# Kernel optimization log

Hardware: AMD Instinct MI355X
Metric: run time of the kernel (lower is better)

The kernel has to match this reference:

```python
import jax, jax.numpy as jnp
import numpy as np

B, MC, U, N, DIN, DOUT, E = 2048, 4, 20000, 100000, 128, 128, 65536
RES_RATE = 0.9


def setup_inputs() -> dict:
    key = jax.random.key(0)
    ks = jax.random.split(key, 12)
    s = 1.0 / np.sqrt(DIN)
    return {
        'nodes': jax.random.randint(ks[0], (B,), 0, N),
        'unique_ids': jax.random.randint(ks[1], (U,), 0, N),
        'row_idx': jnp.repeat(jnp.arange(B), E // B),
        'layer_idx': jax.random.randint(ks[2], (E,), 0, MC),
        'col_idx': jax.random.randint(ks[3], (E,), 0, U),
        'agg_table': jax.random.normal(ks[4], (N, DIN), jnp.float32),
        'ff_table': jax.random.normal(ks[5], (N, DIN), jnp.float32),
        'Wv_agg': jax.random.normal(ks[6], (DIN, DOUT), jnp.float32) * s,
        'Wv_ff': jax.random.normal(ks[7], (DIN, DOUT), jnp.float32) * s,
        'Wk': jax.random.normal(ks[8], (DIN, DOUT), jnp.float32) * s,
        'Wq': jax.random.normal(ks[9], (DIN, DOUT), jnp.float32) * s,
        'mu_w': jax.random.normal(ks[10], (2 * DOUT, 1), jnp.float32) * s,
    }


def reference(nodes, unique_ids, row_idx, layer_idx, col_idx,
              agg_table, ff_table, Wv_agg, Wv_ff, Wk, Wq, mu_w):
    # feature lookups (the 'features' encoder returns (agg_attr, ff_attr))
    embed_agg = agg_table[unique_ids]            # [U, DIN]
    self_agg_raw = agg_table[nodes]              # [B, DIN]
    self_ff_raw = ff_table[nodes]                # [B, DIN]

    # highway K/Q from raw self features
    self_pair = jnp.stack((self_agg_raw, self_ff_raw), axis=1)  # [B, 2, DIN]
    K = self_pair @ Wk                            # [B, 2, DOUT]
    Q = self_pair @ Wq                            # [B, 2, DOUT]

    embed_agg_v = embed_agg @ Wv_agg              # [U, DOUT]
    self_agg = self_agg_raw @ Wv_agg              # [B, DOUT]

    # dense normalized neighbor mask [B, MC, U]
    mask = jnp.zeros((B, MC, U), jnp.float32).at[row_idx, layer_idx, col_idx].set(1.0)
    cnt = mask.sum(-1, keepdims=True)
    mask = mask / jnp.where(cnt == 0, 1.0, cnt)
    neigh = jnp.einsum('bmu,ud->bmd', mask, embed_agg_v)  # [B, MC, DOUT]

    # persona combination
    coef = jnp.concatenate(
        (jnp.broadcast_to(self_agg[:, None, :], (B, MC, DOUT)), neigh), axis=-1)
    norm = jnp.maximum(jnp.linalg.norm(coef, axis=-1, keepdims=True), 1e-12)
    coef = jax.nn.softmax((coef / norm) @ mu_w, axis=1)    # [B, MC, 1]
    neigh_sum = jnp.sum(neigh * coef, axis=1)              # [B, DOUT]
    self_agg = (self_agg + neigh_sum) / 2.0

    # feed-forward branch + highway attention
    self_ff = self_ff_raw @ Wv_ff                          # [B, DOUT]
    V = jnp.stack((self_agg, self_ff), axis=1)             # [B, 2, DOUT]
    scores = jax.nn.softmax(jnp.einsum('bid,bjd->bij', K, Q) / DOUT, axis=-1)
    new = jnp.einsum('bij,bjd->bid', scores, V)            # [B, 2, DOUT]
    self_agg = RES_RATE * self_agg + (1 - RES_RATE) * new[:, 0]
    self_ff = RES_RATE * self_ff + (1 - RES_RATE) * new[:, 1]
    return jax.nn.elu(self_agg), jax.nn.elu(self_ff)
```

## Files before the change

kernel.cpp:

```cpp
#include <hip/hip_runtime.h>
#include <hip/hip_bf16.h>

typedef unsigned short u16;
typedef unsigned int u32;
typedef unsigned long long u64;

#define NB 2048
#define NMC 4
#define NU 20000
#define ND 128
#define EPB 32

typedef __attribute__((ext_vector_type(8))) short bf16x8;
typedef __attribute__((ext_vector_type(4))) float f32x4;

__device__ __forceinline__ u32 pack_bf16(float a, float b) {
    __hip_bfloat162 h = __float22bfloat162_rn(make_float2(a, b));
    return *(u32*)&h;
}
__device__ __forceinline__ u16 f2bf(float f) {
    u32 x = __float_as_uint(f);
    return (u16)((x + 0x7fffu + ((x >> 16) & 1u)) >> 16);
}
__device__ __forceinline__ float wsum(float v) {
    #pragma unroll
    for (int off = 32; off; off >>= 1) v += __shfl_xor(v, off);
    return v;
}

__global__ __launch_bounds__(256) void prep_wt(
    const float* __restrict__ Wv_agg, const float* __restrict__ Wk,
    const float* __restrict__ Wq, const float* __restrict__ Wv_ff,
    u16* __restrict__ WT)
{
    __shared__ float Wl[16 * ND];
    const int m = blockIdx.x >> 3;
    const int ks = (blockIdx.x & 7) * 16;
    const int t = threadIdx.x;

    const float* W = (m == 0) ? Wv_agg : (m == 1) ? Wk : (m == 2) ? Wq : Wv_ff;
    const float4* src = (const float4*)(W + ks * ND);
    float4* dst = (float4*)Wl;
    dst[t * 2] = src[t * 2];
    dst[t * 2 + 1] = src[t * 2 + 1];
    __syncthreads();

    const int c = t >> 1, kh = t & 1;
    float v[8];
    #pragma unroll
    for (int j = 0; j < 8; j++) v[j] = Wl[(kh * 8 + j) * ND + c];
    uint4 pk;
    pk.x = pack_bf16(v[0], v[1]);
    pk.y = pack_bf16(v[2], v[3]);
    pk.z = pack_bf16(v[4], v[5]);
    pk.w = pack_bf16(v[6], v[7]);
    *(uint4*)&WT[((size_t)(m * ND + c)) * ND + ks + kh * 8] = pk;
}

#define LDSK 72
#define EMBED_BLOCKS 157

__global__ __launch_bounds__(256) void gemm_all(
    const float* __restrict__ agg, const float* __restrict__ ff,
    const u16* __restrict__ WT,
    const int* __restrict__ uids, const int* __restrict__ nodes,
    u16* __restrict__ embed_bf,
    float* __restrict__ selfA, float* __restrict__ selfF,
    float* __restrict__ K0, float* __restrict__ K1,
    float* __restrict__ Q0, float* __restrict__ Q1)
{
    __shared__ u16 As[ND * LDSK];
    __shared__ u16 Bs[ND * LDSK];

    const int bx = blockIdx.x;
    const int t  = threadIdx.x;

    const float* table = agg; const int* ids = uids; int wtm = 0;
    float* outf = nullptr; u16* outb = nullptr;
    int M, r0;
    if (bx < EMBED_BLOCKS) {
        M = NU; r0 = bx * 128; outb = embed_bf;
    } else {
        int z = bx - EMBED_BLOCKS;
        int mode = z >> 4;
        r0 = (z & 15) * 128;
        M = NB; ids = nodes;
        switch (mode) {
            case 0: table = agg; wtm = 0; outf = selfA; break;
            case 1: table = agg; wtm = 1; outf = K0;    break;
            case 2: table = agg; wtm = 2; outf = Q0;    break;
            case 3: table = ff;  wtm = 3; outf = selfF; break;
            case 4: table = ff;  wtm = 1; outf = K1;    break;
            default: table = ff; wtm = 2; outf = Q1;    break;
        }
    }

    const int rs = t >> 1, hs = t & 1;
    int srow = r0 + rs;
    const int id = ids[srow < M ? srow : (M - 1)];
    const float* arow = table + (size_t)id * ND;
    const u16* wrow = WT + ((size_t)(wtm * ND + rs)) * ND;

    const int w = t >> 6, lane = t & 63, q = lane >> 4, li = lane & 15;

    f32x4 acc[2][8];
    #pragma unroll
    for (int i = 0; i < 2; i++)
        #pragma unroll
        for (int j = 0; j < 8; j++) acc[i][j] = (f32x4){0.f, 0.f, 0.f, 0.f};

    for (int pass = 0; pass < 2; pass++) {
        const int k0 = pass * 64;
        {
            const float4* asrc = (const float4*)(arow + k0 + hs * 32);
            #pragma unroll
            for (int i = 0; i < 4; i++) {
                float4 v0 = asrc[2 * i], v1 = asrc[2 * i + 1];
                uint4 pk;
                pk.x = pack_bf16(v0.x, v0.y);
                pk.y = pack_bf16(v0.z, v0.w);
                pk.z = pack_bf16(v1.x, v1.y);
                pk.w = pack_bf16(v1.z, v1.w);
                *(uint4*)&As[rs * LDSK + hs * 32 + i * 8] = pk;
            }
        }
        {
            const uint4* bsrc = (const uint4*)(wrow + k0 + hs * 32);
            #pragma unroll
            for (int i = 0; i < 4; i++)
                *(uint4*)&Bs[rs * LDSK + hs * 32 + i * 8] = bsrc[i];
        }
        __syncthreads();

        #pragma unroll
        for (int c = 0; c < 2; c++) {
            const int kk = c * 32 + q * 8;
            bf16x8 af[2], bfr[8];
            #pragma unroll
            for (int tr = 0; tr < 2; tr++)
                af[tr] = *(const bf16x8*)&As[(w * 32 + tr * 16 + li) * LDSK + kk];
            #pragma unroll
            for (int tc = 0; tc < 8; tc++)
                bfr[tc] = *(const bf16x8*)&Bs[(tc * 16 + li) * LDSK + kk];
            #pragma unroll
            for (int tr = 0; tr < 2; tr++)
                #pragma unroll
                for (int tc = 0; tc < 8; tc++)
                    acc[tr][tc] = __builtin_amdgcn_mfma_f32_16x16x32_bf16(
                        af[tr], bfr[tc], acc[tr][tc], 0, 0, 0);
        }
        __syncthreads();
    }

    #pragma unroll
    for (int tr = 0; tr < 2; tr++) {
        const int rloc = w * 32 + tr * 16 + q * 4;
        #pragma unroll
        for (int r = 0; r < 4; r++) {
            const int row = r0 + rloc + r;
            if (row < M) {
                if (outb) {
                    #pragma unroll
                    for (int tc = 0; tc < 8; tc++)
                        outb[(size_t)row * ND + tc * 16 + li] = f2bf(acc[tr][tc][r]);
                } else {
                    #pragma unroll
                    for (int tc = 0; tc < 8; tc++)
                        outf[(size_t)row * ND + tc * 16 + li] = acc[tr][tc][r];
                }
            }
        }
    }
}

__global__ __launch_bounds__(64) void finalize(
    const int* __restrict__ layer_idx, const int* __restrict__ col_idx,
    const u16* __restrict__ embed_bf,
    const float* __restrict__ selfA, const float* __restrict__ selfF,
    const float* __restrict__ K0, const float* __restrict__ K1,
    const float* __restrict__ Q0, const float* __restrict__ Q1,
    const float* __restrict__ mu_w, float* __restrict__ out)
{
    const int b = blockIdx.x;
    const int t = threadIdx.x;

    int l = 0, c = 0;
    if (t < EPB) {
        l = layer_idx[b * EPB + t];
        c = col_idx[b * EPB + t];
    }
    const u32 key = ((u32)l << 15) | (u32)c;
    int dup = 0;
    #pragma unroll
    for (int j = 0; j < EPB; j++) {
        u32 kj = __shfl(key, j);
        dup |= (j < t && kj == key);
    }
    const int keep = (t < EPB) && !dup;
    float inv[NMC];
    #pragma unroll
    for (int m = 0; m < NMC; m++) {
        int cm = __popcll(__ballot(keep && (l == m)));
        inv[m] = cm > 0 ? 1.f / (float)cm : 0.f;
    }
    const u32 info = ((u32)c << 3) | ((u32)l << 1) | (u32)keep;

    float a0x = 0.f, a0y = 0.f, a1x = 0.f, a1y = 0.f;
    float a2x = 0.f, a2y = 0.f, a3x = 0.f, a3y = 0.f;
    #pragma unroll
    for (int e = 0; e < EPB; e++) {
        u32 inf = __shfl(info, e);
        if (inf & 1u) {
            int ce = inf >> 3, le = (inf >> 1) & 3;
            u32 v = *(const u32*)&embed_bf[(size_t)ce * ND + 2 * t];
            float lo = __uint_as_float(v << 16);
            float hi = __uint_as_float(v & 0xffff0000u);
            switch (le) {
                case 0: a0x += lo; a0y += hi; break;
                case 1: a1x += lo; a1y += hi; break;
                case 2: a2x += lo; a2y += hi; break;
                default: a3x += lo; a3y += hi; break;
            }
        }
    }
    const float n0x = a0x * inv[0], n0y = a0y * inv[0];
    const float n1x = a1x * inv[1], n1y = a1y * inv[1];
    const float n2x = a2x * inv[2], n2y = a2y * inv[2];
    const float n3x = a3x * inv[3], n3y = a3y * inv[3];

    const size_t base2 = (size_t)b * ND + 2 * t;
    float2 sA = *(const float2*)&selfA[base2];
    float2 sF = *(const float2*)&selfF[base2];
    float2 k0 = *(const float2*)&K0[base2];
    float2 k1 = *(const float2*)&K1[base2];
    float2 q0 = *(const float2*)&Q0[base2];
    float2 q1 = *(const float2*)&Q1[base2];
    float2 mu0 = *(const float2*)&mu_w[2 * t];
    float2 mu1 = *(const float2*)&mu_w[ND + 2 * t];

    const float sn = wsum(sA.x * sA.x + sA.y * sA.y);
    const float ds = wsum(sA.x * mu0.x + sA.y * mu0.y);
    float nn[NMC], dn[NMC];
    nn[0] = wsum(n0x * n0x + n0y * n0y); dn[0] = wsum(n0x * mu1.x + n0y * mu1.y);
    nn[1] = wsum(n1x * n1x + n1y * n1y); dn[1] = wsum(n1x * mu1.x + n1y * mu1.y);
    nn[2] = wsum(n2x * n2x + n2y * n2y); dn[2] = wsum(n2x * mu1.x + n2y * mu1.y);
    nn[3] = wsum(n3x * n3x + n3y * n3y); dn[3] = wsum(n3x * mu1.x + n3y * mu1.y);
    const float s00 = wsum(k0.x * q0.x + k0.y * q0.y) * (1.f / 128.f);
    const float s01 = wsum(k0.x * q1.x + k0.y * q1.y) * (1.f / 128.f);
    const float s10 = wsum(k1.x * q0.x + k1.y * q0.y) * (1.f / 128.f);
    const float s11 = wsum(k1.x * q1.x + k1.y * q1.y) * (1.f / 128.f);

    float sc[NMC], mx = -1e30f;
    #pragma unroll
    for (int m = 0; m < NMC; m++) {
        float nrm = fmaxf(sqrtf(sn + nn[m]), 1e-12f);
        sc[m] = (ds + dn[m]) / nrm;
        mx = fmaxf(mx, sc[m]);
    }
    float se = 0.f, ee[NMC];
    #pragma unroll
    for (int m = 0; m < NMC; m++) { ee[m] = expf(sc[m] - mx); se += ee[m]; }
    const float ise = 1.f / se;
    const float bc0 = ee[0] * ise, bc1 = ee[1] * ise;
    const float bc2 = ee[2] * ise, bc3 = ee[3] * ise;

    const float m0 = fmaxf(s00, s01), e00 = expf(s00 - m0), e01 = expf(s01 - m0);
    const float id0 = 1.f / (e00 + e01);
    const float c00 = e00 * id0, c01 = e01 * id0;
    const float m1 = fmaxf(s10, s11), e10 = expf(s10 - m1), e11 = expf(s11 - m1);
    const float id1 = 1.f / (e10 + e11);
    const float c10 = e10 * id1, c11 = e11 * id1;

    const float nsx = n0x * bc0 + n1x * bc1 + n2x * bc2 + n3x * bc3;
    const float nsy = n0y * bc0 + n1y * bc1 + n2y * bc2 + n3y * bc3;
    const float sa1x = (sA.x + nsx) * 0.5f, sa1y = (sA.y + nsy) * 0.5f;
    float o0x = 0.9f * sa1x + 0.1f * (c00 * sa1x + c01 * sF.x);
    float o0y = 0.9f * sa1y + 0.1f * (c00 * sa1y + c01 * sF.y);
    float o1x = 0.9f * sF.x + 0.1f * (c10 * sa1x + c11 * sF.x);
    float o1y = 0.9f * sF.y + 0.1f * (c10 * sa1y + c11 * sF.y);
    o0x = o0x > 0.f ? o0x : (expf(o0x) - 1.f);
    o0y = o0y > 0.f ? o0y : (expf(o0y) - 1.f);
    o1x = o1x > 0.f ? o1x : (expf(o1x) - 1.f);
    o1y = o1y > 0.f ? o1y : (expf(o1y) - 1.f);
    *(float2*)&out[base2] = make_float2(o0x, o0y);
    *(float2*)&out[(size_t)NB * ND + base2] = make_float2(o1x, o1y);
}

extern "C" void kernel_launch(void* const* d_in, const int* in_sizes, int n_in,
                              void* d_out, int out_size, void* d_ws, size_t ws_size,
                              hipStream_t stream) {
    const int* nodes  = (const int*)d_in[0];
    const int* uids   = (const int*)d_in[1];
    const int* layer  = (const int*)d_in[3];
    const int* col    = (const int*)d_in[4];
    const float* agg    = (const float*)d_in[5];
    const float* ff     = (const float*)d_in[6];
    const float* Wv_agg = (const float*)d_in[7];
    const float* Wv_ff  = (const float*)d_in[8];
    const float* Wk     = (const float*)d_in[9];
    const float* Wq     = (const float*)d_in[10];
    const float* mu     = (const float*)d_in[11];

    u16*   WT       = (u16*)d_ws;
    u16*   embed_bf = WT + (size_t)4 * ND * ND;
    float* fbase    = (float*)(embed_bf + (size_t)NU * ND);
    float* selfA = fbase;
    float* selfF = selfA + (size_t)NB * ND;
    float* K0    = selfF + (size_t)NB * ND;
    float* K1    = K0 + (size_t)NB * ND;
    float* Q0    = K1 + (size_t)NB * ND;
    float* Q1    = Q0 + (size_t)NB * ND;

    float* out = (float*)d_out;

    prep_wt<<<32, 256, 0, stream>>>(Wv_agg, Wk, Wq, Wv_ff, WT);

    gemm_all<<<EMBED_BLOCKS + 6 * (NB / 128), 256, 0, stream>>>(
        agg, ff, WT, uids, nodes,
        embed_bf, selfA, selfF, K0, K1, Q0, Q1);

    finalize<<<NB, 64, 0, stream>>>(
        layer, col, embed_bf, selfA, selfF, K0, K1, Q0, Q1, mu, out);
}
```

Measured before the change: 153.2 us.

## Fuse weight transpose into GEMM and load A fragments directly into registers

```diff
diff --git a/kernel.cpp b/kernel.cpp
--- a/kernel.cpp
+++ b/kernel.cpp
@@ -3,13 +3,13 @@
 
 typedef unsigned short u16;
 typedef unsigned int u32;
-typedef unsigned long long u64;
 
 #define NB 2048
 #define NMC 4
 #define NU 20000
 #define ND 128
 #define EPB 32
+#define LDW 136
 
 typedef __attribute__((ext_vector_type(8))) short bf16x8;
 typedef __attribute__((ext_vector_type(4))) float f32x4;
@@ -28,54 +28,24 @@
     return v;
 }
 
-__global__ __launch_bounds__(256) void prep_wt(
-    const float* __restrict__ Wv_agg, const float* __restrict__ Wk,
-    const float* __restrict__ Wq, const float* __restrict__ Wv_ff,
-    u16* __restrict__ WT)
-{
-    __shared__ float Wl[16 * ND];
-    const int m = blockIdx.x >> 3;
-    const int ks = (blockIdx.x & 7) * 16;
-    const int t = threadIdx.x;
-
-    const float* W = (m == 0) ? Wv_agg : (m == 1) ? Wk : (m == 2) ? Wq : Wv_ff;
-    const float4* src = (const float4*)(W + ks * ND);
-    float4* dst = (float4*)Wl;
-    dst[t * 2] = src[t * 2];
-    dst[t * 2 + 1] = src[t * 2 + 1];
-    __syncthreads();
-
-    const int c = t >> 1, kh = t & 1;
-    float v[8];
-    #pragma unroll
-    for (int j = 0; j < 8; j++) v[j] = Wl[(kh * 8 + j) * ND + c];
-    uint4 pk;
-    pk.x = pack_bf16(v[0], v[1]);
-    pk.y = pack_bf16(v[2], v[3]);
-    pk.z = pack_bf16(v[4], v[5]);
-    pk.w = pack_bf16(v[6], v[7]);
-    *(uint4*)&WT[((size_t)(m * ND + c)) * ND + ks + kh * 8] = pk;
-}
-
-#define LDSK 72
 #define EMBED_BLOCKS 157
 
 __global__ __launch_bounds__(256) void gemm_all(
     const float* __restrict__ agg, const float* __restrict__ ff,
-    const u16* __restrict__ WT,
+    const float* __restrict__ Wv_agg, const float* __restrict__ Wv_ff,
+    const float* __restrict__ Wk, const float* __restrict__ Wq,
     const int* __restrict__ uids, const int* __restrict__ nodes,
     u16* __restrict__ embed_bf,
     float* __restrict__ selfA, float* __restrict__ selfF,
     float* __restrict__ K0, float* __restrict__ K1,
     float* __restrict__ Q0, float* __restrict__ Q1)
 {
-    __shared__ u16 As[ND * LDSK];
-    __shared__ u16 Bs[ND * LDSK];
+    __shared__ u16 WTl[ND * LDW];
 
     const int bx = blockIdx.x;
     const int t  = threadIdx.x;
 
-    const float* table = agg; const int* ids = uids; int wtm = 0;
+    const float* table = agg; const int* ids = uids; const float* W = Wv_agg;
     float* outf = nullptr; u16* outb = nullptr;
     int M, r0;
     if (bx < EMBED_BLOCKS) {
@@ -86,22 +56,55 @@
         r0 = (z & 15) * 128;
         M = NB; ids = nodes;
         switch (mode) {
-            case 0: table = agg; wtm = 0; outf = selfA; break;
-            case 1: table = agg; wtm = 1; outf = K0;    break;
-            case 2: table = agg; wtm = 2; outf = Q0;    break;
-            case 3: table = ff;  wtm = 3; outf = selfF; break;
-            case 4: table = ff;  wtm = 1; outf = K1;    break;
-            default: table = ff; wtm = 2; outf = Q1;    break;
-        }
-    }
-
-    const int rs = t >> 1, hs = t & 1;
-    int srow = r0 + rs;
-    const int id = ids[srow < M ? srow : (M - 1)];
-    const float* arow = table + (size_t)id * ND;
-    const u16* wrow = WT + ((size_t)(wtm * ND + rs)) * ND;
+            case 0: table = agg; W = Wv_agg; outf = selfA; break;
+            case 1: table = agg; W = Wk;     outf = K0;    break;
+            case 2: table = agg; W = Wq;     outf = Q0;    break;
+            case 3: table = ff;  W = Wv_ff;  outf = selfF; break;
+            case 4: table = ff;  W = Wk;     outf = K1;    break;
+            default: table = ff; W = Wq;     outf = Q1;    break;
+        }
+    }
+
+    {
+        const int kr = t >> 1;
+        const int nh = t & 1;
+        const float4* wsrc = (const float4*)(W + kr * ND + nh * 64);
+        #pragma unroll
+        for (int i = 0; i < 16; i++) {
+            float4 v = wsrc[i];
+            int n = nh * 64 + i * 4;
+            WTl[(n + 0) * LDW + kr] = f2bf(v.x);
+            WTl[(n + 1) * LDW + kr] = f2bf(v.y);
+            WTl[(n + 2) * LDW + kr] = f2bf(v.z);
+            WTl[(n + 3) * LDW + kr] = f2bf(v.w);
+        }
+    }
 
     const int w = t >> 6, lane = t & 63, q = lane >> 4, li = lane & 15;
+    const int rbase = r0 + w * 32;
+    int ra = rbase + li;      ra = ra < M ? ra : M - 1;
+    int rb = rbase + 16 + li; rb = rb < M ? rb : M - 1;
+    const float* arow0 = table + (size_t)ids[ra] * ND + q * 8;
+    const float* arow1 = table + (size_t)ids[rb] * ND + q * 8;
+
+    bf16x8 af[2][4];
+    #pragma unroll
+    for (int c = 0; c < 4; c++) {
+        float4 v0 = *(const float4*)(arow0 + c * 32);
+        float4 v1 = *(const float4*)(arow0 + c * 32 + 4);
+        uint4 pk;
+        pk.x = pack_bf16(v0.x, v0.y); pk.y = pack_bf16(v0.z, v0.w);
+        pk.z = pack_bf16(v1.x, v1.y); pk.w = pack_bf16(v1.z, v1.w);
+        af[0][c] = *(bf16x8*)&pk;
+        float4 u0 = *(const float4*)(arow1 + c * 32);
+        float4 u1 = *(const float4*)(arow1 + c * 32 + 4);
+        uint4 qk;
+        qk.x = pack_bf16(u0.x, u0.y); qk.y = pack_bf16(u0.z, u0.w);
+        qk.z = pack_bf16(u1.x, u1.y); qk.w = pack_bf16(u1.z, u1.w);
+        af[1][c] = *(bf16x8*)&qk;
+    }
+
+    __syncthreads();
 
     f32x4 acc[2][8];
     #pragma unroll
@@ -109,47 +112,21 @@
         #pragma unroll
         for (int j = 0; j < 8; j++) acc[i][j] = (f32x4){0.f, 0.f, 0.f, 0.f};
 
-    for (int pass = 0; pass < 2; pass++) {
-        const int k0 = pass * 64;
-        {
-            const float4* asrc = (const float4*)(arow + k0 + hs * 32);
-            #pragma unroll
-            for (int i = 0; i < 4; i++) {
-                float4 v0 = asrc[2 * i], v1 = asrc[2 * i + 1];
-                uint4 pk;
-                pk.x = pack_bf16(v0.x, v0.y);
-                pk.y = pack_bf16(v0.z, v0.w);
-                pk.z = pack_bf16(v1.x, v1.y);
-                pk.w = pack_bf16(v1.z, v1.w);
-                *(uint4*)&As[rs * LDSK + hs * 32 + i * 8] = pk;
-            }
-        }
-        {
-            const uint4* bsrc = (const uint4*)(wrow + k0 + hs * 32);
-            #pragma unroll
-            for (int i = 0; i < 4; i++)
-                *(uint4*)&Bs[rs * LDSK + hs * 32 + i * 8] = bsrc[i];
-        }
-        __syncthreads();
-
-        #pragma unroll
-        for (int c = 0; c < 2; c++) {
-            const int kk = c * 32 + q * 8;
-            bf16x8 af[2], bfr[8];
-            #pragma unroll
-            for (int tr = 0; tr < 2; tr++)
-                af[tr] = *(const bf16x8*)&As[(w * 32 + tr * 16 + li) * LDSK + kk];
-            #pragma unroll
-            for (int tc = 0; tc < 8; tc++)
-                bfr[tc] = *(const bf16x8*)&Bs[(tc * 16 + li) * LDSK + kk];
-            #pragma unroll
-            for (int tr = 0; tr < 2; tr++)
-                #pragma unroll
-                for (int tc = 0; tc < 8; tc++)
-                    acc[tr][tc] = __builtin_amdgcn_mfma_f32_16x16x32_bf16(
-                        af[tr], bfr[tc], acc[tr][tc], 0, 0, 0);
-        }
-        __syncthreads();
+    #pragma unroll 2
+    for (int tc = 0; tc < 8; tc++) {
+        const u16* bp = &WTl[(tc * 16 + li) * LDW + q * 8];
+        bf16x8 b0 = *(const bf16x8*)(bp);
+        bf16x8 b1 = *(const bf16x8*)(bp + 32);
+        bf16x8 b2 = *(const bf16x8*)(bp + 64);
+        bf16x8 b3 = *(const bf16x8*)(bp + 96);
+        acc[0][tc] = __builtin_amdgcn_mfma_f32_16x16x32_bf16(af[0][0], b0, acc[0][tc], 0, 0, 0);
+        acc[1][tc] = __builtin_amdgcn_mfma_f32_16x16x32_bf16(af[1][0], b0, acc[1][tc], 0, 0, 0);
+        acc[0][tc] = __builtin_amdgcn_mfma_f32_16x16x32_bf16(af[0][1], b1, acc[0][tc], 0, 0, 0);
+        acc[1][tc] = __builtin_amdgcn_mfma_f32_16x16x32_bf16(af[1][1], b1, acc[1][tc], 0, 0, 0);
+        acc[0][tc] = __builtin_amdgcn_mfma_f32_16x16x32_bf16(af[0][2], b2, acc[0][tc], 0, 0, 0);
+        acc[1][tc] = __builtin_amdgcn_mfma_f32_16x16x32_bf16(af[1][2], b2, acc[1][tc], 0, 0, 0);
+        acc[0][tc] = __builtin_amdgcn_mfma_f32_16x16x32_bf16(af[0][3], b3, acc[0][tc], 0, 0, 0);
+        acc[1][tc] = __builtin_amdgcn_mfma_f32_16x16x32_bf16(af[1][3], b3, acc[1][tc], 0, 0, 0);
     }
 
     #pragma unroll
@@ -301,8 +278,7 @@
     const float* Wq     = (const float*)d_in[10];
     const float* mu     = (const float*)d_in[11];
 
-    u16*   WT       = (u16*)d_ws;
-    u16*   embed_bf = WT + (size_t)4 * ND * ND;
+    u16*   embed_bf = (u16*)d_ws;
     float* fbase    = (float*)(embed_bf + (size_t)NU * ND);
     float* selfA = fbase;
     float* selfF = selfA + (size_t)NB * ND;
@@ -313,10 +289,8 @@
 
     float* out = (float*)d_out;
 
-    prep_wt<<<32, 256, 0, stream>>>(Wv_agg, Wk, Wq, Wv_ff, WT);
-
     gemm_all<<<EMBED_BLOCKS + 6 * (NB / 128), 256, 0, stream>>>(
-        agg, ff, WT, uids, nodes,
+        agg, ff, Wv_agg, Wv_ff, Wk, Wq, uids, nodes,
         embed_bf, selfA, selfF, K0, K1, Q0, Q1);
 
     finalize<<<NB, 64, 0, stream>>>(
```

After: 166.3 us. 1.09x slower.

## Halve GEMM row tile to 64 and load full K in one pass

Applied to the files above, without the earlier changes.

```diff
diff --git a/kernel.cpp b/kernel.cpp
--- a/kernel.cpp
+++ b/kernel.cpp
@@ -3,13 +3,13 @@
 
 typedef unsigned short u16;
 typedef unsigned int u32;
-typedef unsigned long long u64;
 
 #define NB 2048
 #define NMC 4
 #define NU 20000
 #define ND 128
 #define EPB 32
+#define LDW 136
 
 typedef __attribute__((ext_vector_type(8))) short bf16x8;
 typedef __attribute__((ext_vector_type(4))) float f32x4;
@@ -57,8 +57,7 @@
     *(uint4*)&WT[((size_t)(m * ND + c)) * ND + ks + kh * 8] = pk;
 }
 
-#define LDSK 72
-#define EMBED_BLOCKS 157
+#define EMBED_BLOCKS 313
 
 __global__ __launch_bounds__(256) void gemm_all(
     const float* __restrict__ agg, const float* __restrict__ ff,
@@ -69,8 +68,8 @@
     float* __restrict__ K0, float* __restrict__ K1,
     float* __restrict__ Q0, float* __restrict__ Q1)
 {
-    __shared__ u16 As[ND * LDSK];
-    __shared__ u16 Bs[ND * LDSK];
+    __shared__ u16 As[64 * LDW];
+    __shared__ u16 Bs[ND * LDW];
 
     const int bx = blockIdx.x;
     const int t  = threadIdx.x;
@@ -79,11 +78,11 @@
     float* outf = nullptr; u16* outb = nullptr;
     int M, r0;
     if (bx < EMBED_BLOCKS) {
-        M = NU; r0 = bx * 128; outb = embed_bf;
+        M = NU; r0 = bx * 64; outb = embed_bf;
     } else {
         int z = bx - EMBED_BLOCKS;
-        int mode = z >> 4;
-        r0 = (z & 15) * 128;
+        int mode = z >> 5;
+        r0 = (z & 31) * 64;
         M = NB; ids = nodes;
         switch (mode) {
             case 0: table = agg; wtm = 0; outf = selfA; break;
@@ -95,79 +94,72 @@
         }
     }
 
-    const int rs = t >> 1, hs = t & 1;
-    int srow = r0 + rs;
-    const int id = ids[srow < M ? srow : (M - 1)];
-    const float* arow = table + (size_t)id * ND;
-    const u16* wrow = WT + ((size_t)(wtm * ND + rs)) * ND;
+    {
+        const int rs = t >> 2;
+        const int qs = t & 3;
+        int srow = r0 + rs;
+        const int id = ids[srow < M ? srow : (M - 1)];
+        const float4* asrc = (const float4*)(table + (size_t)id * ND + qs * 32);
+        #pragma unroll
+        for (int i = 0; i < 2; i++) {
+            float4 v0 = asrc[4 * i + 0], v1 = asrc[4 * i + 1];
+            float4 v2 = asrc[4 * i + 2], v3 = asrc[4 * i + 3];
+            uint4 p0, p1;
+            p0.x = pack_bf16(v0.x, v0.y); p0.y = pack_bf16(v0.z, v0.w);
+            p0.z = pack_bf16(v1.x, v1.y); p0.w = pack_bf16(v1.z, v1.w);
+            p1.x = pack_bf16(v2.x, v2.y); p1.y = pack_bf16(v2.z, v2.w);
+            p1.z = pack_bf16(v3.x, v3.y); p1.w = pack_bf16(v3.z, v3.w);
+            *(uint4*)&As[rs * LDW + qs * 32 + i * 16] = p0;
+            *(uint4*)&As[rs * LDW + qs * 32 + i * 16 + 8] = p1;
+        }
+    }
+    {
+        const int cs = t >> 1;
+        const int hs = t & 1;
+        const uint4* bsrc = (const uint4*)(WT + ((size_t)(wtm * ND + cs)) * ND + hs * 64);
+        #pragma unroll
+        for (int i = 0; i < 8; i++)
+            *(uint4*)&Bs[cs * LDW + hs * 64 + i * 8] = bsrc[i];
+    }
+    __syncthreads();
 
     const int w = t >> 6, lane = t & 63, q = lane >> 4, li = lane & 15;
 
-    f32x4 acc[2][8];
-    #pragma unroll
-    for (int i = 0; i < 2; i++)
-        #pragma unroll
-        for (int j = 0; j < 8; j++) acc[i][j] = (f32x4){0.f, 0.f, 0.f, 0.f};
-
-    for (int pass = 0; pass < 2; pass++) {
-        const int k0 = pass * 64;
-        {
-            const float4* asrc = (const float4*)(arow + k0 + hs * 32);
-            #pragma unroll
-            for (int i = 0; i < 4; i++) {
-                float4 v0 = asrc[2 * i], v1 = asrc[2 * i + 1];
-                uint4 pk;
-                pk.x = pack_bf16(v0.x, v0.y);
-                pk.y = pack_bf16(v0.z, v0.w);
-                pk.z = pack_bf16(v1.x, v1.y);
-                pk.w = pack_bf16(v1.z, v1.w);
-                *(uint4*)&As[rs * LDSK + hs * 32 + i * 8] = pk;
-            }
-        }
-        {
-            const uint4* bsrc = (const uint4*)(wrow + k0 + hs * 32);
-            #pragma unroll
-            for (int i = 0; i < 4; i++)
-                *(uint4*)&Bs[rs * LDSK + hs * 32 + i * 8] = bsrc[i];
-        }
-        __syncthreads();
-
-        #pragma unroll
-        for (int c = 0; c < 2; c++) {
-            const int kk = c * 32 + q * 8;
-            bf16x8 af[2], bfr[8];
-            #pragma unroll
-            for (int tr = 0; tr < 2; tr++)
-                af[tr] = *(const bf16x8*)&As[(w * 32 + tr * 16 + li) * LDSK + kk];
-            #pragma unroll
-            for (int tc = 0; tc < 8; tc++)
-                bfr[tc] = *(const bf16x8*)&Bs[(tc * 16 + li) * LDSK + kk];
-            #pragma unroll
-            for (int tr = 0; tr < 2; tr++)
+    bf16x8 af[4];
+    #pragma unroll
+    for (int c = 0; c < 4; c++)
+        af[c] = *(const bf16x8*)&As[(w * 16 + li) * LDW + c * 32 + q * 8];
+
+    f32x4 acc[8];
+    #pragma unroll
+    for (int j = 0; j < 8; j++) acc[j] = (f32x4){0.f, 0.f, 0.f, 0.f};
+
+    #pragma unroll
+    for (int tc = 0; tc < 8; tc++) {
+        const u16* bp = &Bs[(tc * 16 + li) * LDW + q * 8];
+        bf16x8 b0 = *(const bf16x8*)(bp);
+        bf16x8 b1 = *(const bf16x8*)(bp + 32);
+        bf16x8 b2 = *(const bf16x8*)(bp + 64);
+        bf16x8 b3 = *(const bf16x8*)(bp + 96);
+        acc[tc] = __builtin_amdgcn_mfma_f32_16x16x32_bf16(af[0], b0, acc[tc], 0, 0, 0);
+        acc[tc] = __builtin_amdgcn_mfma_f32_16x16x32_bf16(af[1], b1, acc[tc], 0, 0, 0);
+        acc[tc] = __builtin_amdgcn_mfma_f32_16x16x32_bf16(af[2], b2, acc[tc], 0, 0, 0);
+        acc[tc] = __builtin_amdgcn_mfma_f32_16x16x32_bf16(af[3], b3, acc[tc], 0, 0, 0);
+    }
+
+    const int rloc = w * 16 + q * 4;
+    #pragma unroll
+    for (int r = 0; r < 4; r++) {
+        const int row = r0 + rloc + r;
+        if (row < M) {
+            if (outb) {
                 #pragma unroll
                 for (int tc = 0; tc < 8; tc++)
-                    acc[tr][tc] = __builtin_amdgcn_mfma_f32_16x16x32_bf16(
-                        af[tr], bfr[tc], acc[tr][tc], 0, 0, 0);
-        }
-        __syncthreads();
-    }
-
-    #pragma unroll
-    for (int tr = 0; tr < 2; tr++) {
-        const int rloc = w * 32 + tr * 16 + q * 4;
-        #pragma unroll
-        for (int r = 0; r < 4; r++) {
-            const int row = r0 + rloc + r;
-            if (row < M) {
-                if (outb) {
-                    #pragma unroll
-                    for (int tc = 0; tc < 8; tc++)
-                        outb[(size_t)row * ND + tc * 16 + li] = f2bf(acc[tr][tc][r]);
-                } else {
-                    #pragma unroll
-                    for (int tc = 0; tc < 8; tc++)
-                        outf[(size_t)row * ND + tc * 16 + li] = acc[tr][tc][r];
-                }
+                    outb[(size_t)row * ND + tc * 16 + li] = f2bf(acc[tc][r]);
+            } else {
+                #pragma unroll
+                for (int tc = 0; tc < 8; tc++)
+                    outf[(size_t)row * ND + tc * 16 + li] = acc[tc][r];
             }
         }
     }
@@ -315,7 +307,7 @@
 
     prep_wt<<<32, 256, 0, stream>>>(Wv_agg, Wk, Wq, Wv_ff, WT);
 
-    gemm_all<<<EMBED_BLOCKS + 6 * (NB / 128), 256, 0, stream>>>(
+    gemm_all<<<EMBED_BLOCKS + 6 * (NB / 64), 256, 0, stream>>>(
         agg, ff, WT, uids, nodes,
         embed_bf, selfA, selfF, K0, K1, Q0, Q1);
 
```

Result: no change. 154.5 us (+0.9%).
